# Kernel tuning notes

Hardware: AMD Instinct MI355X
Metric: run time of the kernel (lower is better)

The kernel has to match this reference:

```python
import jax, jax.numpy as jnp
import numpy as np


def setup_inputs() -> dict:
    key = jax.random.key(0)
    k1, k2, k3 = jax.random.split(key, 3)
    vol_shape = (4, 1, 128, 192, 192)   # [B, C, D, H, W]
    dsc_shape = (4, 1, 8, 12, 12)       # PatchGAN-style discriminator logits
    return {
        "dsc_fake": jax.random.normal(k1, dsc_shape, dtype=jnp.float32),
        "predicts": jax.random.normal(k2, vol_shape, dtype=jnp.float32),
        "y_data": jax.random.normal(k3, vol_shape, dtype=jnp.float32),
        "zeros": jnp.zeros(dsc_shape, dtype=jnp.float32),
    }


def reference(dsc_fake, predicts, y_data, zeros):
    # BCE with logits (stable form), target = zeros
    bce = jnp.mean(
        jnp.maximum(dsc_fake, 0.0) - dsc_fake * zeros
        + jnp.log1p(jnp.exp(-jnp.abs(dsc_fake)))
    )
    # L1 loss between target volume and prediction
    g_loss_l1 = jnp.mean(jnp.abs(y_data - predicts))
    # Finite-difference gradient MSE along D, H, W (axes 2,3,4).
    # Original detaches to numpy, so this term carries no gradient.
    yd = jax.lax.stop_gradient(y_data)
    pr = jax.lax.stop_gradient(predicts)
    g_loss_gd = jnp.float32(0.0)
    for ax in (2, 3, 4):
        gy = jnp.abs(jnp.gradient(yd, axis=ax))   # central diff interior, one-sided edges
        gp = jnp.abs(jnp.gradient(pr, axis=ax))
        g_loss_gd = g_loss_gd + jnp.mean((gy - gp) ** 2)
    return bce + 100.0 * g_loss_l1 + 100.0 * g_loss_gd
```

## Files before the change

### kernel.cpp

```cpp
#include <hip/hip_runtime.h>
#include <math.h>

namespace {
constexpr int BATCH = 4;
constexpr int DDIM  = 128;
constexpr int HDIM  = 192;
constexpr int WDIM  = 192;
constexpr long long NTOT = (long long)BATCH * DDIM * HDIM * WDIM;
constexpr int NDSC  = 4 * 1 * 8 * 12 * 12;

constexpr int HT     = 4;
constexpr int DT     = 32;
constexpr int ROWS   = HT + 2;
constexpr int SLABF  = ROWS * WDIM;
constexpr int SLAB2  = 2 * SLABF;
constexpr int RING   = 5;
constexpr int UNITS  = (SLAB2 * 4) / 1024;
constexpr int BLOCKV = 64;
constexpr int NHT    = HDIM / HT;
constexpr int NDC    = DDIM / DT;
constexpr int GRIDV  = BATCH * NDC * NHT;
constexpr int PLSTR  = HDIM * WDIM;
constexpr int BLOCKF = 256;
}

#define GTERM(dy, dp, s2) { float t0_ = fabsf(dy) - fabsf(dp); gd = fmaf(t0_ * t0_, (s2), gd); }

#define STAGE(buf, plane)                                                       \
    {                                                                           \
        const int poff_ = (plane) * PLSTR;                                      \
        _Pragma("unroll")                                                       \
        for (int k = 0; k < UNITS; ++k) {                                       \
            __builtin_amdgcn_global_load_lds(                                   \
                (const __attribute__((address_space(1))) void*)(sr[k] + poff_), \
                (__attribute__((address_space(3))) void*)(&slab[buf][k * 256]), \
                16, 0, 0);                                                      \
        }                                                                       \
    }

__global__ __launch_bounds__(BLOCKV) void vol_kernel(const float* __restrict__ p,
                                                     const float* __restrict__ y,
                                                     float* __restrict__ part) {
    __shared__ float slab[RING][SLAB2];

    const int lane = threadIdx.x;
    const int r    = lane >> 4;
    const int i16  = lane & 15;
    const int w0   = i16 * 12;

    const int blk0 = blockIdx.x;
    const int swz  = (blk0 & 7) * (GRIDV / 8) + (blk0 >> 3);
    const int ht   = swz % NHT;
    const int rs   = swz / NHT;
    const int dc   = rs & (NDC - 1);
    const int b    = rs >> 2;
    const int h0   = ht * HT;
    const int d0   = dc * DT;
    const int h    = h0 + r;

    const float* sr[UNITS];
    #pragma unroll
    for (int k = 0; k < UNITS; ++k) {
        const int fi  = k * 256 + lane * 4;
        const int ts  = fi >= SLABF;
        const int fj  = ts ? fi - SLABF : fi;
        const int row = fj / WDIM;
        const int col = fj - row * WDIM;
        int hrow = h0 - 1 + row;
        hrow = hrow < 0 ? 0 : (hrow > HDIM - 1 ? HDIM - 1 : hrow);
        sr[k] = (ts ? p : y) + (b * DDIM * HDIM + hrow) * WDIM + col;
    }

    float4 ym[2][3], yc[2][3];
    {
        const int pmz = d0 ? d0 - 1 : 0;
        const int om = ((b * DDIM + pmz) * HDIM + h) * WDIM + w0;
        const int oc = ((b * DDIM + d0 ) * HDIM + h) * WDIM + w0;
        #pragma unroll
        for (int g = 0; g < 3; ++g) {
            ym[0][g] = *(const float4*)(y + om + 4 * g);
            ym[1][g] = *(const float4*)(p + om + 4 * g);
            yc[0][g] = *(const float4*)(y + oc + 4 * g);
            yc[1][g] = *(const float4*)(p + oc + 4 * g);
        }
    }
    STAGE(0, d0);
    STAGE(1, d0 + 1);
    STAGE(2, d0 + 2);
    STAGE(3, d0 + 3);

    float l1 = 0.f, gd = 0.f;
    const float s2h  = (h == 0 || h == HDIM - 1) ? 1.f : 0.25f;
    const float s2w0 = (i16 == 0)  ? 1.f : 0.25f;
    const float s2w3 = (i16 == 15) ? 1.f : 0.25f;

    int cur = 0;
    #pragma unroll 1
    for (int i = 0; i < DT; ++i) {
        const int e = d0 + i;
        if (i < DT - 2)       { asm volatile("s_waitcnt vmcnt(18)" ::: "memory"); }
        else if (i == DT - 2) { asm volatile("s_waitcnt vmcnt(9)"  ::: "memory"); }
        else                  { asm volatile("s_waitcnt vmcnt(0)"  ::: "memory"); }
        __builtin_amdgcn_sched_barrier(0);

        if (i <= DT - 4) {
            int pl = e + 4; if (pl > DDIM - 1) pl = DDIM - 1;
            const int stg = cur ? cur - 1 : RING - 1;
            STAGE(stg, pl);
        }

        const int nx = (cur + 1 == RING) ? 0 : cur + 1;
        const float* cs = &slab[cur][0];
        const float* ns = &slab[nx][0];
        const float s2d = (e == 0 || e == DDIM - 1) ? 1.f : 0.25f;

        const int rowc = (r + 1) * WDIM;
        const float wlY = cs[rowc + (i16 ? w0 - 1 : 0)];
        const float wrY = cs[rowc + (i16 < 15 ? w0 + 12 : WDIM - 1)];
        const float wlP = cs[SLABF + rowc + (i16 ? w0 - 1 : 0)];
        const float wrP = cs[SLABF + rowc + (i16 < 15 ? w0 + 12 : WDIM - 1)];

        float4 cn[2][3];
        #pragma unroll
        for (int g = 0; g < 3; ++g) {
            const int off = w0 + 4 * g;
            const float4 cny = *(const float4*)&ns[rowc + off];
            const float4 cnp = *(const float4*)&ns[SLABF + rowc + off];
            const float4 hmy = *(const float4*)&cs[r * WDIM + off];
            const float4 hpy = *(const float4*)&cs[(r + 2) * WDIM + off];
            const float4 hmp = *(const float4*)&cs[SLABF + r * WDIM + off];
            const float4 hpp = *(const float4*)&cs[SLABF + (r + 2) * WDIM + off];
            cn[0][g] = cny; cn[1][g] = cnp;
            const float4 ay = yc[0][g], ap = yc[1][g];
            const float4 my = ym[0][g], mp = ym[1][g];

            l1 += fabsf(ay.x - ap.x) + fabsf(ay.y - ap.y)
                + fabsf(ay.z - ap.z) + fabsf(ay.w - ap.w);
            GTERM(hpy.x - hmy.x, hpp.x - hmp.x, s2h);
            GTERM(hpy.y - hmy.y, hpp.y - hmp.y, s2h);
            GTERM(hpy.z - hmy.z, hpp.z - hmp.z, s2h);
            GTERM(hpy.w - hmy.w, hpp.w - hmp.w, s2h);
            GTERM(cny.x - my.x, cnp.x - mp.x, s2d);
            GTERM(cny.y - my.y, cnp.y - mp.y, s2d);
            GTERM(cny.z - my.z, cnp.z - mp.z, s2d);
            GTERM(cny.w - my.w, cnp.w - mp.w, s2d);
        }
        {
            const float4 a0 = yc[0][0], a1 = yc[0][1], a2 = yc[0][2];
            const float4 p0 = yc[1][0], p1 = yc[1][1], p2 = yc[1][2];
            GTERM(a0.y - wlY , p0.y - wlP , s2w0);
            GTERM(a0.z - a0.x, p0.z - p0.x, 0.25f);
            GTERM(a0.w - a0.y, p0.w - p0.y, 0.25f);
            GTERM(a1.x - a0.z, p1.x - p0.z, 0.25f);
            GTERM(a1.y - a0.w, p1.y - p0.w, 0.25f);
            GTERM(a1.z - a1.x, p1.z - p1.x, 0.25f);
            GTERM(a1.w - a1.y, p1.w - p1.y, 0.25f);
            GTERM(a2.x - a1.z, p2.x - p1.z, 0.25f);
            GTERM(a2.y - a1.w, p2.y - p1.w, 0.25f);
            GTERM(a2.z - a2.x, p2.z - p2.x, 0.25f);
            GTERM(a2.w - a2.y, p2.w - p2.y, 0.25f);
            GTERM(wrY  - a2.z, wrP  - p2.z, s2w3);
        }
        #pragma unroll
        for (int g = 0; g < 3; ++g) {
            ym[0][g] = yc[0][g]; ym[1][g] = yc[1][g];
            yc[0][g] = cn[0][g]; yc[1][g] = cn[1][g];
        }
        cur = nx;
    }

    #pragma unroll
    for (int off = 32; off > 0; off >>= 1) {
        l1 += __shfl_down(l1, off, 64);
        gd += __shfl_down(gd, off, 64);
    }
    if (lane == 0) {
        part[2 * blk0]     = l1;
        part[2 * blk0 + 1] = gd;
    }
}

__global__ __launch_bounds__(BLOCKF) void finalize_kernel(const float* __restrict__ dsc,
                                                          const float* __restrict__ part,
                                                          float* __restrict__ out) {
    float l1 = 0.f, gd = 0.f, s = 0.f;
    for (int i = threadIdx.x; i < GRIDV; i += BLOCKF) {
        l1 += part[2 * i];
        gd += part[2 * i + 1];
    }
    for (int i = threadIdx.x; i < NDSC; i += BLOCKF) {
        const float x = dsc[i];
        s += fmaxf(x, 0.f) + log1pf(expf(-fabsf(x)));
    }
    __shared__ float a[4], c[4], e2[4];
    #pragma unroll
    for (int off = 32; off > 0; off >>= 1) {
        l1 += __shfl_down(l1, off, 64);
        gd += __shfl_down(gd, off, 64);
        s  += __shfl_down(s,  off, 64);
    }
    if ((threadIdx.x & 63) == 0) {
        const int w = threadIdx.x >> 6;
        a[w] = l1; c[w] = gd; e2[w] = s;
    }
    __syncthreads();
    if (threadIdx.x == 0) {
        const float bce = (e2[0] + e2[1] + e2[2] + e2[3]) / (float)NDSC;
        const float l1m = (a[0] + a[1] + a[2] + a[3]) / (float)NTOT;
        const float gdm = (c[0] + c[1] + c[2] + c[3]) / (float)NTOT;
        out[0] = bce + 100.f * (l1m + gdm);
    }
}

extern "C" void kernel_launch(void* const* d_in, const int* in_sizes, int n_in,
                              void* d_out, int out_size, void* d_ws, size_t ws_size,
                              hipStream_t stream) {
    const float* dsc_fake = (const float*)d_in[0];
    const float* predicts = (const float*)d_in[1];
    const float* y_data   = (const float*)d_in[2];
    float* part = (float*)d_ws;
    float* out  = (float*)d_out;

    vol_kernel<<<GRIDV, BLOCKV, 0, stream>>>(predicts, y_data, part);
    finalize_kernel<<<1, BLOCKF, 0, stream>>>(dsc_fake, part, out);
}
```

Before: 196.0 us.

## Replace LDS ring-buffer staging with register streaming and cross-lane shuffles

Drops the LDS slab ring fed by global_load_lds. Each wave now streams its own rows straight into registers, with one-plane-ahead prefetch through inline asm loads. H and W neighbours come from wave shuffles, and only the halo row above or below each 4-row group is loaded separately. Blocks grow to 4 waves covering 16 rows over 8 depth planes, with an LDS reduction across waves. This removes LDS traffic and ring bookkeeping, but the prefetch depth is shallower (a full vmcnt(0) wait every plane) and halo reloads are redundant.

Result: slower. 354.4 us (+80.8%).

```diff
diff --git a/kernel.cpp b/kernel.cpp
--- a/kernel.cpp
+++ b/kernel.cpp
@@ -9,145 +9,138 @@
 constexpr long long NTOT = (long long)BATCH * DDIM * HDIM * WDIM;
 constexpr int NDSC  = 4 * 1 * 8 * 12 * 12;
 
-constexpr int HT     = 4;
-constexpr int DT     = 32;
-constexpr int ROWS   = HT + 2;
-constexpr int SLABF  = ROWS * WDIM;
-constexpr int SLAB2  = 2 * SLABF;
-constexpr int RING   = 5;
-constexpr int UNITS  = (SLAB2 * 4) / 1024;
-constexpr int BLOCKV = 64;
-constexpr int NHT    = HDIM / HT;
+constexpr int DT     = 8;
 constexpr int NDC    = DDIM / DT;
-constexpr int GRIDV  = BATCH * NDC * NHT;
+constexpr int HB     = 16;
+constexpr int NHB    = HDIM / HB;
+constexpr int BLOCKV = 256;
+constexpr int GRIDV  = BATCH * NDC * NHB;
 constexpr int PLSTR  = HDIM * WDIM;
 constexpr int BLOCKF = 256;
 }
 
 #define GTERM(dy, dp, s2) { float t0_ = fabsf(dy) - fabsf(dp); gd = fmaf(t0_ * t0_, (s2), gd); }
 
-#define STAGE(buf, plane)                                                       \
-    {                                                                           \
-        const int poff_ = (plane) * PLSTR;                                      \
-        _Pragma("unroll")                                                       \
-        for (int k = 0; k < UNITS; ++k) {                                       \
-            __builtin_amdgcn_global_load_lds(                                   \
-                (const __attribute__((address_space(1))) void*)(sr[k] + poff_), \
-                (__attribute__((address_space(3))) void*)(&slab[buf][k * 256]), \
-                16, 0, 0);                                                      \
-        }                                                                       \
-    }
-
-__global__ __launch_bounds__(BLOCKV) void vol_kernel(const float* __restrict__ p,
-                                                     const float* __restrict__ y,
-                                                     float* __restrict__ part) {
-    __shared__ float slab[RING][SLAB2];
-
-    const int lane = threadIdx.x;
+#define ALOAD3(d0_, d1_, d2_, ap_)                                   \
+    asm volatile("global_load_dwordx4 %0, %3, off\n\t"               \
+                 "global_load_dwordx4 %1, %3, off offset:16\n\t"     \
+                 "global_load_dwordx4 %2, %3, off offset:32"         \
+                 : "=&v"(d0_), "=&v"(d1_), "=&v"(d2_)                \
+                 : "v"((const void*)(ap_)))
+
+__device__ __forceinline__ float4 shup16(float4 v) {
+    float4 r;
+    r.x = __shfl_up(v.x, 16, 64); r.y = __shfl_up(v.y, 16, 64);
+    r.z = __shfl_up(v.z, 16, 64); r.w = __shfl_up(v.w, 16, 64);
+    return r;
+}
+__device__ __forceinline__ float4 shdn16(float4 v) {
+    float4 r;
+    r.x = __shfl_down(v.x, 16, 64); r.y = __shfl_down(v.y, 16, 64);
+    r.z = __shfl_down(v.z, 16, 64); r.w = __shfl_down(v.w, 16, 64);
+    return r;
+}
+__device__ __forceinline__ float4 sel4(bool c, float4 a, float4 b) {
+    float4 r;
+    r.x = c ? a.x : b.x; r.y = c ? a.y : b.y;
+    r.z = c ? a.z : b.z; r.w = c ? a.w : b.w;
+    return r;
+}
+
+__global__ __launch_bounds__(BLOCKV, 3) void vol_kernel(const float* __restrict__ p,
+                                                        const float* __restrict__ y,
+                                                        float* __restrict__ part) {
+    const int tid  = threadIdx.x;
+    const int wv   = tid >> 6;
+    const int lane = tid & 63;
     const int r    = lane >> 4;
     const int i16  = lane & 15;
     const int w0   = i16 * 12;
 
     const int blk0 = blockIdx.x;
     const int swz  = (blk0 & 7) * (GRIDV / 8) + (blk0 >> 3);
-    const int ht   = swz % NHT;
-    const int rs   = swz / NHT;
-    const int dc   = rs & (NDC - 1);
-    const int b    = rs >> 2;
-    const int h0   = ht * HT;
+    const int hb   = swz % NHB;
+    const int rest = swz / NHB;
+    const int dc   = rest % NDC;
+    const int b    = rest / NDC;
+    const int h0w  = hb * HB + wv * 4;
+    const int h    = h0w + r;
     const int d0   = dc * DT;
-    const int h    = h0 + r;
-
-    const float* sr[UNITS];
-    #pragma unroll
-    for (int k = 0; k < UNITS; ++k) {
-        const int fi  = k * 256 + lane * 4;
-        const int ts  = fi >= SLABF;
-        const int fj  = ts ? fi - SLABF : fi;
-        const int row = fj / WDIM;
-        const int col = fj - row * WDIM;
-        int hrow = h0 - 1 + row;
-        hrow = hrow < 0 ? 0 : (hrow > HDIM - 1 ? HDIM - 1 : hrow);
-        sr[k] = (ts ? p : y) + (b * DDIM * HDIM + hrow) * WDIM + col;
-    }
-
-    float4 ym[2][3], yc[2][3];
+    const int rb   = (r < 2) ? (h0w > 0 ? h0w - 1 : 0)
+                             : (h0w + 4 < HDIM ? h0w + 4 : HDIM - 1);
+
+    const long long base  = (long long)(b * DDIM) * PLSTR;
+    const long long rowO  = base + (long long)h  * WDIM + w0;
+    const long long rowB  = base + (long long)rb * WDIM + w0;
+
+    float4 ymY[3], ymP[3], ycY[3], ycP[3], bmY[3], bmP[3];
     {
-        const int pmz = d0 ? d0 - 1 : 0;
-        const int om = ((b * DDIM + pmz) * HDIM + h) * WDIM + w0;
-        const int oc = ((b * DDIM + d0 ) * HDIM + h) * WDIM + w0;
+        const int pm = d0 ? d0 - 1 : 0;
         #pragma unroll
         for (int g = 0; g < 3; ++g) {
-            ym[0][g] = *(const float4*)(y + om + 4 * g);
-            ym[1][g] = *(const float4*)(p + om + 4 * g);
-            yc[0][g] = *(const float4*)(y + oc + 4 * g);
-            yc[1][g] = *(const float4*)(p + oc + 4 * g);
-        }
-    }
-    STAGE(0, d0);
-    STAGE(1, d0 + 1);
-    STAGE(2, d0 + 2);
-    STAGE(3, d0 + 3);
+            ymY[g] = *(const float4*)(y + rowO + (long long)pm * PLSTR + 4 * g);
+            ymP[g] = *(const float4*)(p + rowO + (long long)pm * PLSTR + 4 * g);
+            ycY[g] = *(const float4*)(y + rowO + (long long)d0 * PLSTR + 4 * g);
+            ycP[g] = *(const float4*)(p + rowO + (long long)d0 * PLSTR + 4 * g);
+            bmY[g] = *(const float4*)(y + rowB + (long long)d0 * PLSTR + 4 * g);
+            bmP[g] = *(const float4*)(p + rowB + (long long)d0 * PLSTR + 4 * g);
+        }
+    }
+    float4 cnY[3], cnP[3], bnY[3], bnP[3];
+    {
+        const long long po = (long long)(d0 + 1) * PLSTR;
+        ALOAD3(cnY[0], cnY[1], cnY[2], y + rowO + po);
+        ALOAD3(cnP[0], cnP[1], cnP[2], p + rowO + po);
+        ALOAD3(bnY[0], bnY[1], bnY[2], y + rowB + po);
+        ALOAD3(bnP[0], bnP[1], bnP[2], p + rowB + po);
+    }
 
     float l1 = 0.f, gd = 0.f;
     const float s2h  = (h == 0 || h == HDIM - 1) ? 1.f : 0.25f;
     const float s2w0 = (i16 == 0)  ? 1.f : 0.25f;
     const float s2w3 = (i16 == 15) ? 1.f : 0.25f;
 
-    int cur = 0;
     #pragma unroll 1
     for (int i = 0; i < DT; ++i) {
         const int e = d0 + i;
-        if (i < DT - 2)       { asm volatile("s_waitcnt vmcnt(18)" ::: "memory"); }
-        else if (i == DT - 2) { asm volatile("s_waitcnt vmcnt(9)"  ::: "memory"); }
-        else                  { asm volatile("s_waitcnt vmcnt(0)"  ::: "memory"); }
+        asm volatile("s_waitcnt vmcnt(0)" ::: "memory");
         __builtin_amdgcn_sched_barrier(0);
 
-        if (i <= DT - 4) {
-            int pl = e + 4; if (pl > DDIM - 1) pl = DDIM - 1;
-            const int stg = cur ? cur - 1 : RING - 1;
-            STAGE(stg, pl);
-        }
-
-        const int nx = (cur + 1 == RING) ? 0 : cur + 1;
-        const float* cs = &slab[cur][0];
-        const float* ns = &slab[nx][0];
         const float s2d = (e == 0 || e == DDIM - 1) ? 1.f : 0.25f;
 
-        const int rowc = (r + 1) * WDIM;
-        const float wlY = cs[rowc + (i16 ? w0 - 1 : 0)];
-        const float wrY = cs[rowc + (i16 < 15 ? w0 + 12 : WDIM - 1)];
-        const float wlP = cs[SLABF + rowc + (i16 ? w0 - 1 : 0)];
-        const float wrP = cs[SLABF + rowc + (i16 < 15 ? w0 + 12 : WDIM - 1)];
-
-        float4 cn[2][3];
+        float wlY = __shfl_up (ycY[2].w, 1, 64);
+        float wrY = __shfl_down(ycY[0].x, 1, 64);
+        float wlP = __shfl_up (ycP[2].w, 1, 64);
+        float wrP = __shfl_down(ycP[0].x, 1, 64);
+        wlY = (i16 == 0)  ? ycY[0].x : wlY;  wlP = (i16 == 0)  ? ycP[0].x : wlP;
+        wrY = (i16 == 15) ? ycY[2].w : wrY;  wrP = (i16 == 15) ? ycP[2].w : wrP;
+
         #pragma unroll
         for (int g = 0; g < 3; ++g) {
-            const int off = w0 + 4 * g;
-            const float4 cny = *(const float4*)&ns[rowc + off];
-            const float4 cnp = *(const float4*)&ns[SLABF + rowc + off];
-            const float4 hmy = *(const float4*)&cs[r * WDIM + off];
-            const float4 hpy = *(const float4*)&cs[(r + 2) * WDIM + off];
-            const float4 hmp = *(const float4*)&cs[SLABF + r * WDIM + off];
-            const float4 hpp = *(const float4*)&cs[SLABF + (r + 2) * WDIM + off];
-            cn[0][g] = cny; cn[1][g] = cnp;
-            const float4 ay = yc[0][g], ap = yc[1][g];
-            const float4 my = ym[0][g], mp = ym[1][g];
+            const float4 ay = ycY[g], ap = ycP[g];
+            const float4 my = ymY[g], mp = ymP[g];
+            const float4 ny = cnY[g], np2 = cnP[g];
 
             l1 += fabsf(ay.x - ap.x) + fabsf(ay.y - ap.y)
                 + fabsf(ay.z - ap.z) + fabsf(ay.w - ap.w);
+
+            const float4 hmy = sel4(r == 0, bmY[g], shup16(ay));
+            const float4 hmp = sel4(r == 0, bmP[g], shup16(ap));
+            const float4 hpy = sel4(r == 3, bmY[g], shdn16(ay));
+            const float4 hpp = sel4(r == 3, bmP[g], shdn16(ap));
             GTERM(hpy.x - hmy.x, hpp.x - hmp.x, s2h);
             GTERM(hpy.y - hmy.y, hpp.y - hmp.y, s2h);
             GTERM(hpy.z - hmy.z, hpp.z - hmp.z, s2h);
             GTERM(hpy.w - hmy.w, hpp.w - hmp.w, s2h);
-            GTERM(cny.x - my.x, cnp.x - mp.x, s2d);
-            GTERM(cny.y - my.y, cnp.y - mp.y, s2d);
-            GTERM(cny.z - my.z, cnp.z - mp.z, s2d);
-            GTERM(cny.w - my.w, cnp.w - mp.w, s2d);
+
+            GTERM(ny.x - my.x, np2.x - mp.x, s2d);
+            GTERM(ny.y - my.y, np2.y - mp.y, s2d);
+            GTERM(ny.z - my.z, np2.z - mp.z, s2d);
+            GTERM(ny.w - my.w, np2.w - mp.w, s2d);
         }
         {
-            const float4 a0 = yc[0][0], a1 = yc[0][1], a2 = yc[0][2];
-            const float4 p0 = yc[1][0], p1 = yc[1][1], p2 = yc[1][2];
+            const float4 a0 = ycY[0], a1 = ycY[1], a2 = ycY[2];
+            const float4 p0 = ycP[0], p1 = ycP[1], p2 = ycP[2];
             GTERM(a0.y - wlY , p0.y - wlP , s2w0);
             GTERM(a0.z - a0.x, p0.z - p0.x, 0.25f);
             GTERM(a0.w - a0.y, p0.w - p0.y, 0.25f);
@@ -161,22 +154,34 @@
             GTERM(a2.w - a2.y, p2.w - p2.y, 0.25f);
             GTERM(wrY  - a2.z, wrP  - p2.z, s2w3);
         }
+
         #pragma unroll
         for (int g = 0; g < 3; ++g) {
-            ym[0][g] = yc[0][g]; ym[1][g] = yc[1][g];
-            yc[0][g] = cn[0][g]; yc[1][g] = cn[1][g];
-        }
-        cur = nx;
-    }
-
+            ymY[g] = ycY[g]; ymP[g] = ycP[g];
+            ycY[g] = cnY[g]; ycP[g] = cnP[g];
+            bmY[g] = bnY[g]; bmP[g] = bnP[g];
+        }
+        if (i < DT - 1) {
+            int pl = e + 2; if (pl > DDIM - 1) pl = DDIM - 1;
+            const long long po = (long long)pl * PLSTR;
+            ALOAD3(cnY[0], cnY[1], cnY[2], y + rowO + po);
+            ALOAD3(cnP[0], cnP[1], cnP[2], p + rowO + po);
+            ALOAD3(bnY[0], bnY[1], bnY[2], y + rowB + po);
+            ALOAD3(bnP[0], bnP[1], bnP[2], p + rowB + po);
+        }
+    }
+
+    __shared__ float red1[4], red2[4];
     #pragma unroll
     for (int off = 32; off > 0; off >>= 1) {
         l1 += __shfl_down(l1, off, 64);
         gd += __shfl_down(gd, off, 64);
     }
-    if (lane == 0) {
-        part[2 * blk0]     = l1;
-        part[2 * blk0 + 1] = gd;
+    if (lane == 0) { red1[wv] = l1; red2[wv] = gd; }
+    __syncthreads();
+    if (tid == 0) {
+        part[2 * blk0]     = red1[0] + red1[1] + red1[2] + red1[3];
+        part[2 * blk0 + 1] = red2[0] + red2[1] + red2[2] + red2[3];
     }
 }
 
```
